# Kernel optimization log

Measured on AMD Instinct MI355X. Metric: run time of the kernel, lower is better.

The kernel has to match this reference:

```python
import jax, jax.numpy as jnp
import numpy as np
from jax import lax

DIM = 64        # Branch(dim)
OUT = 2048      # TimesBlock out_channels == TTT model_dim
NH = 8          # num_heads
HD = OUT // NH  # 256 head dim
INNER = 4 * HD  # ttt_mlp hidden
MB = 10         # mini_batch_size
BASE_LR = 0.1   # ttt_base_lr
NK = 6          # TimesBlock num_kernels (k = 1,3,5,7,9,11)
LN_EPS = 1e-6


def _gelu(x):
    return jax.nn.gelu(x, approximate=False)


def _gelu_bwd(x):
    return 0.5 * (1.0 + lax.erf(x / jnp.sqrt(2.0))) + x * jnp.exp(-0.5 * x * x) / jnp.sqrt(2.0 * jnp.pi)


def _ttt_head(qs, ks, vs, W1h, b1h, W2h, b2h, gw, gb):
    # qs/ks/vs: [NC, MB, HD]; sequential scan over mini-batch chunks (TTT inner GD)
    eta = BASE_LR / MB

    def step(carry, chunk):
        W1c, b1c, W2c, b2c = carry
        xq, xk, xv = chunk
        Z1 = xk @ W1c + b1c              # [MB, INNER]
        A1 = _gelu(Z1)
        Z2 = A1 @ W2c + b2c              # [MB, HD]
        # grad of 0.5*||LN(Z2) - (xv - xk)||^2 wrt Z2 (fused LN l2 backward)
        tgt = xv - xk
        mu = Z2.mean(-1, keepdims=True)
        std = jnp.sqrt(Z2.var(-1, keepdims=True) + LN_EPS)
        xhat = (2 * 0 + Z2 - mu) / std
        gout = (gw * xhat + gb) - tgt
        gxh = gout * gw
        gZ2 = (gxh - gxh.mean(-1, keepdims=True) - xhat * (gxh * xhat).mean(-1, keepdims=True)) / std
        gZ1 = (gZ2 @ W2c.T) * _gelu_bwd(Z1)
        # inner-model SGD step
        W1n = W1c - eta * (xk.T @ gZ1)
        b1n = b1c - eta * gZ1.sum(0)
        W2n = W2c - eta * (A1.T @ gZ2)
        b2n = b2c - eta * gZ2.sum(0)
        # apply updated inner model to queries, post-LN + residual
        Z1q = xq @ W1n + b1n
        Z2q = _gelu(Z1q) @ W2n + b2n
        muq = Z2q.mean(-1, keepdims=True)
        stdq = jnp.sqrt(Z2q.var(-1, keepdims=True) + LN_EPS)
        out = xq + gw * ((Z2q - muq) / stdq) + gb
        return (W1n, b1n, W2n, b2n), out

    _, outs = lax.scan(step, (W1h, b1h, W2h, b2h), (qs, ks, vs))
    return outs.reshape(-1, HD)  # [T, HD]


def _forward(x, seg, conv_ws, conv_bs, wq, wk, wv, wo, W1, b1, W2, b2, ln_w, ln_b):
    B, T, C = x.shape
    xg = jnp.transpose(x, (0, 2, 1)).reshape(B, C, T // seg, seg)
    dn = ('NCHW', 'OIHW', 'NCHW')
    acc = 0.0
    for w, bc in zip(conv_ws, conv_bs):
        acc = acc + lax.conv_general_dilated(xg, w, (1, 1), 'SAME', dimension_numbers=dn) + bc[None, :, None, None]
    xb = acc / float(len(conv_ws))            # TimesBlock: mean over kernel ensemble
    xb = jax.nn.silu(xb)
    xb = jnp.transpose(xb.reshape(B, OUT, T), (0, 2, 1))  # [B, T, OUT]

    def heads(h):  # [B,T,OUT] -> [B,NH,NC,MB,HD]
        return jnp.transpose(h.reshape(B, T, NH, HD), (0, 2, 1, 3)).reshape(B, NH, T // MB, MB, HD)

    q = heads(xb @ wq.T)
    k = heads(xb @ wk.T)
    v = heads(xb @ wv.T)
    f = jax.vmap(jax.vmap(_ttt_head, in_axes=(0, 0, 0, 0, 0, 0, 0, 0, 0)),
                 in_axes=(0, 0, 0, None, None, None, None, None, None))
    o = f(q, k, v, W1, b1, W2, b2, ln_w, ln_b)  # [B, NH, T, HD]
    o = jnp.transpose(o, (0, 2, 1, 3)).reshape(B, T, OUT)
    return o @ wo.T


def setup_inputs() -> dict:
    key = jax.random.key(0)
    ks = jax.random.split(key, 24)
    B, T = 2, 400
    inp = {"x": jax.random.normal(ks[0], (B, T, DIM), jnp.float32), "seg": 20}
    for i in range(NK):
        kk = 2 * i + 1
        fan_out = OUT * kk * kk
        inp[f"conv_w{i}"] = jax.random.normal(ks[1 + i], (OUT, DIM, kk, kk), jnp.float32) * np.sqrt(2.0 / fan_out)
        inp[f"conv_b{i}"] = jnp.zeros((OUT,), jnp.float32)
    for j, nm in enumerate(["wq", "wk", "wv", "wo"]):
        inp[nm] = jax.random.normal(ks[8 + j], (OUT, OUT), jnp.float32) * 0.02
    inp["W1"] = jax.random.normal(ks[12], (NH, HD, INNER), jnp.float32) * 0.02
    inp["b1"] = jnp.zeros((NH, INNER), jnp.float32)
    inp["W2"] = jax.random.normal(ks[13], (NH, INNER, HD), jnp.float32) * 0.02
    inp["b2"] = jnp.zeros((NH, HD), jnp.float32)
    inp["ln_w"] = jnp.ones((NH, HD), jnp.float32)
    inp["ln_b"] = jnp.zeros((NH, HD), jnp.float32)
    return inp


def reference(x, seg, conv_w0, conv_b0, conv_w1, conv_b1, conv_w2, conv_b2,
              conv_w3, conv_b3, conv_w4, conv_b4, conv_w5, conv_b5,
              wq, wk, wv, wo, W1, b1, W2, b2, ln_w, ln_b):
    conv_ws = [conv_w0, conv_w1, conv_w2, conv_w3, conv_w4, conv_w5]
    conv_bs = [conv_b0, conv_b1, conv_b2, conv_b3, conv_b4, conv_b5]
    return _forward(x, seg, conv_ws, conv_bs, wq, wk, wv, wo, W1, b1, W2, b2, ln_w, ln_b)
```

## Files before the change

kernel.cpp:

```cpp
#include <hip/hip_runtime.h>


typedef __bf16 bf16x8 __attribute__((ext_vector_type(8)));
typedef float  f32x4  __attribute__((ext_vector_type(4)));

__device__ __forceinline__ unsigned short f2bf(float f){
  unsigned int u = __builtin_bit_cast(unsigned int, f);
  u += 0x7fffu + ((u >> 16) & 1u);
  return (unsigned short)(u >> 16);
}
__device__ __forceinline__ float bf2f(unsigned short b){
  unsigned int u = ((unsigned int)b) << 16;
  return __builtin_bit_cast(float, u);
}
__device__ __forceinline__ float gelu_f(float x){
  return 0.5f * x * (1.0f + erff(x * 0.70710678118654752f));
}
__device__ __forceinline__ float gelu_bwd_f(float x){
  return 0.5f * (1.0f + erff(x * 0.70710678118654752f))
       + x * __expf(-0.5f * x * x) * 0.3989422804014327f;
}


__global__ __launch_bounds__(256) void k_weff(
    const float* __restrict__ w0, const float* __restrict__ w1,
    const float* __restrict__ w2, const float* __restrict__ w3,
    const float* __restrict__ w4, const float* __restrict__ w5,
    unsigned short* __restrict__ weff)
{
  extern __shared__ float sw[];
  const int off[6] = {0, 64, 640, 2240, 5376, 10560};
  const float* ws6[6] = {w0, w1, w2, w3, w4, w5};
  int o = blockIdx.x, tid = threadIdx.x;
#pragma unroll
  for (int i = 0; i < 6; i++){
    int kk = 2 * i + 1, sz = 64 * kk * kk;
    const float* src = ws6[i] + (size_t)o * sz;
    for (int idx = tid; idx < sz; idx += 256) sw[off[i] + idx] = src[idx];
  }
  __syncthreads();
  for (int t = tid; t < 7744; t += 256){
    int c = t / 121, dd = t % 121, di = dd / 11, dj = dd % 11;
    float s = 0.f;
#pragma unroll
    for (int i = 0; i < 6; i++){
      int kk = 2 * i + 1;
      int a = di - 5 + i, b = dj - 5 + i;
      if (a >= 0 && a < kk && b >= 0 && b < kk)
        s += sw[off[i] + (c * kk + a) * kk + b];
    }
    weff[(size_t)o * 7744 + t] = f2bf(s);
  }
}

__global__ __launch_bounds__(256) void k_im2col(
    const float* __restrict__ x, unsigned short* __restrict__ P)
{
  int idx = blockIdx.x * 256 + threadIdx.x;
  if (idx >= 800 * 7744) return;
  int n = idx / 7744, k = idx % 7744;
  int c = k / 121, dd = k % 121, di = dd / 11, dj = dd % 11;
  int b = n / 400, pos = n % 400, i = pos / 20, j = pos % 20;
  int ii = i + di - 5, jj = j + dj - 5;
  float v = 0.f;
  if (ii >= 0 && ii < 20 && jj >= 0 && jj < 20)
    v = x[((size_t)b * 400 + ii * 20 + jj) * 64 + c];
  P[idx] = f2bf(v);
}

__global__ __launch_bounds__(256) void k_wqkv(
    const float* __restrict__ wq, const float* __restrict__ wk,
    const float* __restrict__ wv, unsigned short* __restrict__ dst)
{
  int idx = blockIdx.x * 256 + threadIdx.x;
  if (idx >= 6144 * 2048) return;
  int m = idx >> 11, kk = idx & 2047;
  const float* src = (m < 2048) ? wq : ((m < 4096) ? wk : wv);
  dst[idx] = f2bf(src[(size_t)(m & 2047) * 2048 + kk]);
}

__global__ __launch_bounds__(256) void k_f2bf_copy(
    const float* __restrict__ src, unsigned short* __restrict__ dst, int n)
{
  int idx = blockIdx.x * 256 + threadIdx.x;
  if (idx < n) dst[idx] = f2bf(src[idx]);
}

__global__ __launch_bounds__(256) void k_bsum(
    const float* __restrict__ b0, const float* __restrict__ b1,
    const float* __restrict__ b2, const float* __restrict__ b3,
    const float* __restrict__ b4, const float* __restrict__ b5,
    float* __restrict__ bsum)
{
  int idx = blockIdx.x * 256 + threadIdx.x;
  if (idx < 2048)
    bsum[idx] = b0[idx] + b1[idx] + b2[idx] + b3[idx] + b4[idx] + b5[idx];
}

__global__ __launch_bounds__(256) void k_comb_silu(
    const float* __restrict__ p0, const float* __restrict__ p1,
    const float* __restrict__ bsum, unsigned short* __restrict__ xb)
{
  int i4 = (blockIdx.x * 256 + threadIdx.x) * 4;
  float4 a = *(const float4*)&p0[i4];
  float4 b = *(const float4*)&p1[i4];
  int mm = i4 & 2047;
  float4 bs = *(const float4*)&bsum[mm];
  float v[4] = {a.x + b.x + bs.x, a.y + b.y + bs.y, a.z + b.z + bs.z, a.w + b.w + bs.w};
  ushort4 o;
#pragma unroll
  for (int i = 0; i < 4; i++){
    float t = v[i] * (1.0f / 6.0f);
    float sv = t / (1.0f + __expf(-t));
    ((unsigned short*)&o)[i] = f2bf(sv);
  }
  *(ushort4*)&xb[i4] = o;
}

__global__ __launch_bounds__(256) void k_comb_add4(
    const float* __restrict__ p, float* __restrict__ out)
{
  int i4 = (blockIdx.x * 256 + threadIdx.x) * 4;
  float4 a = *(const float4*)&p[i4];
  float4 b = *(const float4*)&p[1638400 + i4];
  float4 c = *(const float4*)&p[3276800 + i4];
  float4 d = *(const float4*)&p[4915200 + i4];
  float4 o = {a.x + b.x + c.x + d.x, a.y + b.y + c.y + d.y,
              a.z + b.z + c.z + d.z, a.w + b.w + c.w + d.w};
  *(float4*)&out[i4] = o;
}

template<int MODE>
__global__ __launch_bounds__(256, 1) void k_gemm(
    const unsigned short* __restrict__ A, const unsigned short* __restrict__ B,
    int M, int N, int lda, int ldb, int kLen,
    unsigned short* __restrict__ qb, unsigned short* __restrict__ kb,
    unsigned short* __restrict__ vb, float* __restrict__ outf)
{
  __shared__ unsigned short As[128 * 32];
  __shared__ unsigned short Bs[128 * 32];
  int tid = threadIdx.x, w = tid >> 6, l = tid & 63, qd = l >> 4, lm = l & 15;
  int m0 = blockIdx.x * 128, n0 = blockIdx.y * 128;
  int kBase = blockIdx.z * kLen;

  f32x4 acc[4][4];
#pragma unroll
  for (int i = 0; i < 4; i++)
#pragma unroll
    for (int j = 0; j < 4; j++){ acc[i][j][0]=0.f; acc[i][j][1]=0.f; acc[i][j][2]=0.f; acc[i][j][3]=0.f; }

  int nk = kLen >> 5;
  for (int kt = 0; kt < nk; kt++){
    int k0 = kBase + (kt << 5);
#pragma unroll
    for (int i = 0; i < 2; i++){
      int cidx = tid + i * 256;
      int row = cidx >> 2, kc = (cidx & 3) << 3;
      *(uint4*)&As[row * 32 + kc] = *(const uint4*)&A[(size_t)(m0 + row) * lda + k0 + kc];
      int br = n0 + row; if (br >= N) br = N - 1;
      *(uint4*)&Bs[row * 32 + kc] = *(const uint4*)&B[(size_t)br * ldb + k0 + kc];
    }
    __syncthreads();
    bf16x8 af[4], bfv[4];
#pragma unroll
    for (int i = 0; i < 4; i++)
      af[i] = *(const bf16x8*)&As[((w >> 1) * 64 + i * 16 + lm) * 32 + qd * 8];
#pragma unroll
    for (int j = 0; j < 4; j++)
      bfv[j] = *(const bf16x8*)&Bs[((w & 1) * 64 + j * 16 + lm) * 32 + qd * 8];
#pragma unroll
    for (int i = 0; i < 4; i++)
#pragma unroll
      for (int j = 0; j < 4; j++)
        acc[i][j] = __builtin_amdgcn_mfma_f32_16x16x32_bf16(af[i], bfv[j], acc[i][j], 0, 0, 0);
    __syncthreads();
  }

#pragma unroll
  for (int i = 0; i < 4; i++){
    int mBase = m0 + (w >> 1) * 64 + i * 16 + qd * 4;
#pragma unroll
    for (int j = 0; j < 4; j++){
      int n = n0 + (w & 1) * 64 + j * 16 + lm;
      if (n < N){
#pragma unroll
        for (int rr = 0; rr < 4; rr++){
          float val = acc[i][j][rr];
          int mm = mBase + rr;
          if (MODE == 1){
            int proj = mm >> 11, o = mm & 2047, hh = o >> 8, d = o & 255;
            int bh = (n / 400) * 8 + hh, tt = n % 400;
            unsigned short* dst = (proj == 0) ? qb : ((proj == 1) ? kb : vb);
            dst[((size_t)bh * 400 + tt) * 256 + d] = f2bf(val);
          } else {
            outf[(size_t)blockIdx.z * M * N + (size_t)n * M + mm] = val;
          }
        }
      }
    }
  }
}

#define O_W1BT 0
#define O_W2K  16896
#define O_W2N  33792
#define O_XKQ  52224
#define O_TGT  54864
#define O_A1   57424
#define O_A1T  58144
#define O_GZ2  60192
#define O_GZ1  62832
#define O_XQ2  64880
#define O_GZ2T 67520
#define O_XKT  73664
#define O_A1Q  79808
#define O_F32  80528
#define O_GW   81168
#define O_GB   81424
#define US_TOTAL 81680
#define TTT_LDS_BYTES (81680 * 2)

#define A1T_IDX(r, c) (O_A1T + ((((r) * 32) + (c)) ^ (((r) & 3) << 3)))
#define GZ1_IDX(r, c) (O_GZ1 + ((((r) * 32) + (c)) ^ (((r) & 3) << 3)))

#define ETA 0.01f
#define BAR_STRIDE 32
#define PPAR 655360

__global__ __launch_bounds__(256, 1) void k_ttt(
    const unsigned short* __restrict__ qg, const unsigned short* __restrict__ kg,
    const unsigned short* __restrict__ vg,
    const float* __restrict__ W1g, const float* __restrict__ b1g,
    const float* __restrict__ W2g, const float* __restrict__ b2g,
    const float* __restrict__ gwg, const float* __restrict__ gbg,
    unsigned short* __restrict__ part, unsigned short* __restrict__ zqp,
    unsigned int* __restrict__ bar)
{
  extern __shared__ unsigned short lds[];
  float* ldsf = (float*)&lds[O_F32];

  int tid = threadIdx.x, w = tid >> 6, l = tid & 63, qd = l >> 4, lm = l & 15;
  int bid = blockIdx.x;
  int jj = bid >> 3, xx = bid & 7;
  int h  = xx + 8 * (jj >> 4);
  int sl = jj & 15;
  int hh = h & 7;

  for (int i = tid; i < US_TOTAL; i += 256) lds[i] = 0;
  __syncthreads();

  float w1r[4][4][4];
#pragma unroll
  for (int a = 0; a < 4; a++)
#pragma unroll
    for (int nt = 0; nt < 4; nt++)
#pragma unroll
      for (int rr = 0; rr < 4; rr++)
        w1r[a][nt][rr] = W1g[((size_t)hh * 256 + (4 * w + a) * 16 + qd * 4 + rr) * 1024
                             + sl * 64 + nt * 16 + lm];
  float w2r[16][4];
#pragma unroll
  for (int nt = 0; nt < 16; nt++)
#pragma unroll
    for (int rr = 0; rr < 4; rr++)
      w2r[nt][rr] = W2g[((size_t)hh * 1024 + sl * 64 + w * 16 + qd * 4 + rr) * 256
                        + nt * 16 + lm];
  if (tid < 64)  ldsf[tid] = b1g[hh * 1024 + sl * 64 + tid];
  if (tid < 256){
    ldsf[64 + tid] = b2g[hh * 256 + tid];
    lds[O_GW + tid] = f2bf(gwg[hh * 256 + tid]);
    lds[O_GB + tid] = f2bf(gbg[hh * 256 + tid]);
  }

#define WRITE_W1BF() do { \
  _Pragma("unroll") for (int a = 0; a < 4; a++){ \
    int m0i = (4 * w + a) * 16 + qd * 4; \
    _Pragma("unroll") for (int nt = 0; nt < 4; nt++){ \
      int n = nt * 16 + lm; \
      unsigned int p0 = f2bf(w1r[a][nt][0]) | ((unsigned int)f2bf(w1r[a][nt][1]) << 16); \
      unsigned int p1 = f2bf(w1r[a][nt][2]) | ((unsigned int)f2bf(w1r[a][nt][3]) << 16); \
      *(unsigned int*)&lds[O_W1BT + n * 264 + m0i]     = p0; \
      *(unsigned int*)&lds[O_W1BT + n * 264 + m0i + 2] = p1; \
    } } } while(0)

#define WRITE_W2BF() do { \
  int mB = w * 16 + qd * 4; \
  _Pragma("unroll") for (int nt = 0; nt < 16; nt++){ \
    int n = nt * 16 + lm; \
    _Pragma("unroll") for (int rr = 0; rr < 4; rr++) \
      lds[O_W2K + (mB + rr) * 264 + n] = f2bf(w2r[nt][rr]); \
    unsigned int p0 = f2bf(w2r[nt][0]) | ((unsigned int)f2bf(w2r[nt][1]) << 16); \
    unsigned int p1 = f2bf(w2r[nt][2]) | ((unsigned int)f2bf(w2r[nt][3]) << 16); \
    *(unsigned int*)&lds[O_W2N + n * 72 + mB]     = p0; \
    *(unsigned int*)&lds[O_W2N + n * 72 + mB + 2] = p1; \
  } } while(0)

  const size_t hb2 = (size_t)h * 400 * 256;

  unsigned int kreg[5], vreg[5];

#define LOAD_XK_REGS(NCH) do { \
  const unsigned int* kp = (const unsigned int*)(kg + hb2 + (size_t)(NCH) * 2560); \
  const unsigned int* vp = (const unsigned int*)(vg + hb2 + (size_t)(NCH) * 2560); \
  _Pragma("unroll") for (int i5 = 0; i5 < 5; i5++){ \
    kreg[i5] = kp[i5 * 256 + tid]; \
    vreg[i5] = vp[i5 * 256 + tid]; \
  } } while(0)

#define COMMIT_XK_TGT() do { \
  _Pragma("unroll") for (int i5 = 0; i5 < 5; i5++){ \
    int f2i = i5 * 256 + tid; \
    unsigned int ku = kreg[i5], vu = vreg[i5]; \
    int row = f2i >> 7, col = (f2i & 127) * 2; \
    *(unsigned int*)&lds[O_XKQ + row * 264 + col] = ku; \
    lds[O_XKT + col * 24 + row]       = (unsigned short)(ku & 0xffffu); \
    lds[O_XKT + (col + 1) * 24 + row] = (unsigned short)(ku >> 16); \
    float kv0 = bf2f((unsigned short)(ku & 0xffffu)), kv1 = bf2f((unsigned short)(ku >> 16)); \
    float vv0 = bf2f((unsigned short)(vu & 0xffffu)), vv1 = bf2f((unsigned short)(vu >> 16)); \
    unsigned int tu = (unsigned int)f2bf(vv0 - kv0) | ((unsigned int)f2bf(vv1 - kv1) << 16); \
    *(unsigned int*)&lds[O_TGT + row * 256 + col] = tu; \
  } } while(0)

#define LOAD_XQ(NCH) do { \
  const unsigned int* qp = (const unsigned int*)(qg + hb2 + (size_t)(NCH) * 2560); \
  _Pragma("unroll") for (int i5 = 0; i5 < 5; i5++){ \
    int f2i = i5 * 256 + tid; \
    unsigned int qu = qp[f2i]; \
    int row = f2i >> 7, col = (f2i & 127) * 2; \
    *(unsigned int*)&lds[O_XQ2 + row * 264 + col] = qu; \
  } } while(0)

  WRITE_W1BF();
  WRITE_W2BF();
  LOAD_XK_REGS(0);
  COMMIT_XK_TGT();
  LOAD_XQ(0);
  __syncthreads();

  for (int nch = 0; nch < 40; nch++){
    bf16x8 w1f[8];
#pragma unroll
    for (int ks = 0; ks < 8; ks++)
      w1f[ks] = *(const bf16x8*)&lds[O_W1BT + (w * 16 + lm) * 264 + ks * 32 + qd * 8];
    float b1n = ldsf[w * 16 + lm];

    f32x4 z1a; z1a[0]=0.f; z1a[1]=0.f; z1a[2]=0.f; z1a[3]=0.f;
#pragma unroll
    for (int ks = 0; ks < 8; ks++){
      bf16x8 av = *(const bf16x8*)&lds[O_XKQ + lm * 264 + ks * 32 + qd * 8];
      z1a = __builtin_amdgcn_mfma_f32_16x16x32_bf16(av, w1f[ks], z1a, 0, 0, 0);
    }
    float z1v[4];
#pragma unroll
    for (int rr = 0; rr < 4; rr++){
      z1v[rr] = z1a[rr] + b1n;
      int mr = qd * 4 + rr;
      if (mr < 10){
        float a1 = gelu_f(z1v[rr]);
        unsigned short ab = f2bf(a1);
        lds[O_A1 + mr * 72 + w * 16 + lm] = ab;
        lds[A1T_IDX(w * 16 + lm, mr)] = ab;
      }
    }
    __syncthreads();

    bf16x8 a1f[2], w2f[4][2];
#pragma unroll
    for (int ks = 0; ks < 2; ks++)
      a1f[ks] = *(const bf16x8*)&lds[O_A1 + lm * 72 + ks * 32 + qd * 8];
#pragma unroll
    for (int nt4 = 0; nt4 < 4; nt4++)
#pragma unroll
      for (int ks = 0; ks < 2; ks++)
        w2f[nt4][ks] = *(const bf16x8*)&lds[O_W2N + ((4 * w + nt4) * 16 + lm) * 72 + ks * 32 + qd * 8];

    {
      unsigned short* pslot = part + ((nch & 1) ? PPAR : 0) + (size_t)(h * 16 + sl) * 2560;
#pragma unroll
      for (int nt4 = 0; nt4 < 4; nt4++){
        int nt = 4 * w + nt4;
        f32x4 p; p[0]=0.f; p[1]=0.f; p[2]=0.f; p[3]=0.f;
#pragma unroll
        for (int ks = 0; ks < 2; ks++)
          p = __builtin_amdgcn_mfma_f32_16x16x32_bf16(a1f[ks], w2f[nt4][ks], p, 0, 0, 0);
#pragma unroll
        for (int rr = 0; rr < 4; rr++){
          int mr = qd * 4 + rr;
          if (mr < 10)
            __hip_atomic_store(&pslot[mr * 256 + nt * 16 + lm], f2bf(p[rr]),
                               __ATOMIC_RELAXED, __HIP_MEMORY_SCOPE_AGENT);
        }
      }
    }
    __syncthreads();

    if (tid == 0)
      __hip_atomic_fetch_add(bar + h * BAR_STRIDE, 1u, __ATOMIC_RELAXED, __HIP_MEMORY_SCOPE_AGENT);

    if (nch + 1 < 40)
      LOAD_XK_REGS(nch + 1);

    if (nch > 0){
      f32x4 zq; zq[0]=0.f; zq[1]=0.f; zq[2]=0.f; zq[3]=0.f;
#pragma unroll
      for (int ks = 0; ks < 8; ks++){
        bf16x8 av = *(const bf16x8*)&lds[O_XQ2 + lm * 264 + ks * 32 + qd * 8];
        zq = __builtin_amdgcn_mfma_f32_16x16x32_bf16(av, w1f[ks], zq, 0, 0, 0);
      }
#pragma unroll
      for (int rr = 0; rr < 4; rr++){
        int mr = qd * 4 + rr;
        if (mr < 10)
          lds[O_A1Q + mr * 72 + w * 16 + lm] = f2bf(gelu_f(zq[rr] + b1n));
      }
    }
    __syncthreads();

    if (nch > 0){
      LOAD_XQ(nch);
      unsigned short* zq_out = zqp + ((size_t)(h * 16 + sl) * 40 + (nch - 1)) * 2560;
      bf16x8 a1qf[2];
#pragma unroll
      for (int ks = 0; ks < 2; ks++)
        a1qf[ks] = *(const bf16x8*)&lds[O_A1Q + lm * 72 + ks * 32 + qd * 8];
#pragma unroll
      for (int nt4 = 0; nt4 < 4; nt4++){
        int nt = 4 * w + nt4;
        f32x4 p; p[0]=0.f; p[1]=0.f; p[2]=0.f; p[3]=0.f;
#pragma unroll
        for (int ks = 0; ks < 2; ks++)
          p = __builtin_amdgcn_mfma_f32_16x16x32_bf16(a1qf[ks], w2f[nt4][ks], p, 0, 0, 0);
        float bb = (sl == 0) ? ldsf[64 + nt * 16 + lm] : 0.f;
#pragma unroll
        for (int rr = 0; rr < 4; rr++){
          int mr = qd * 4 + rr;
          if (mr < 10)
            zq_out[mr * 256 + nt * 16 + lm] = f2bf(p[rr] + bb);
        }
      }
    }

    if (tid == 0){
      unsigned int target = 16u * (unsigned int)(nch + 1);
      unsigned int spins = 0;
      while (__hip_atomic_load(bar + h * BAR_STRIDE, __ATOMIC_RELAXED, __HIP_MEMORY_SCOPE_AGENT) < target
             && spins < 8000000u){ spins++; __builtin_amdgcn_s_sleep(1); }
    }
    __syncthreads();

    {
      const unsigned long long* pb = (const unsigned long long*)
          (part + ((nch & 1) ? PPAR : 0) + (size_t)h * 16 * 2560);
      for (int r2 = w; r2 < 10; r2 += 4){
        int c0 = l * 4;
        float zz[4];
#pragma unroll
        for (int i = 0; i < 4; i++) zz[i] = ldsf[64 + c0 + i];
#pragma unroll
        for (int s16 = 0; s16 < 16; s16++){
          unsigned long long u = __hip_atomic_load(&pb[(size_t)s16 * 640 + r2 * 64 + l],
                                                   __ATOMIC_RELAXED, __HIP_MEMORY_SCOPE_AGENT);
          zz[0] += bf2f((unsigned short)(u & 0xffffu));
          zz[1] += bf2f((unsigned short)((u >> 16) & 0xffffu));
          zz[2] += bf2f((unsigned short)((u >> 32) & 0xffffu));
          zz[3] += bf2f((unsigned short)(u >> 48));
        }
        float s1 = 0.f, s2 = 0.f;
#pragma unroll
        for (int i = 0; i < 4; i++){ s1 += zz[i]; s2 += zz[i] * zz[i]; }
#pragma unroll
        for (int off = 32; off >= 1; off >>= 1){ s1 += __shfl_xor(s1, off, 64); s2 += __shfl_xor(s2, off, 64); }
        float mu = s1 * (1.f / 256.f);
        float var = s2 * (1.f / 256.f) - mu * mu;
        float rstd = rsqrtf(var + 1e-6f);
        float xh[4], gx[4];
        float t1 = 0.f, t2 = 0.f;
#pragma unroll
        for (int i = 0; i < 4; i++){
          xh[i] = (zz[i] - mu) * rstd;
          float gwv = bf2f(lds[O_GW + c0 + i]), gbv = bf2f(lds[O_GB + c0 + i]);
          float tg = bf2f(lds[O_TGT + r2 * 256 + c0 + i]);
          float go = gwv * xh[i] + gbv - tg;
          gx[i] = go * gwv;
          t1 += gx[i]; t2 += gx[i] * xh[i];
        }
#pragma unroll
        for (int off = 32; off >= 1; off >>= 1){ t1 += __shfl_xor(t1, off, 64); t2 += __shfl_xor(t2, off, 64); }
        float m1 = t1 * (1.f / 256.f), m2 = t2 * (1.f / 256.f);
        float g0 = (gx[0] - m1 - xh[0] * m2) * rstd;
        float g1 = (gx[1] - m1 - xh[1] * m2) * rstd;
        float g2 = (gx[2] - m1 - xh[2] * m2) * rstd;
        float g3 = (gx[3] - m1 - xh[3] * m2) * rstd;
        unsigned int p0 = f2bf(g0) | ((unsigned int)f2bf(g1) << 16);
        unsigned int p1 = f2bf(g2) | ((unsigned int)f2bf(g3) << 16);
        *(unsigned int*)&lds[O_GZ2 + r2 * 264 + c0]     = p0;
        *(unsigned int*)&lds[O_GZ2 + r2 * 264 + c0 + 2] = p1;
      }
    }
    __syncthreads();

    {
      float sum = 0.f;
#pragma unroll
      for (int r2 = 0; r2 < 10; r2++){
        unsigned short g = lds[O_GZ2 + r2 * 264 + tid];
        lds[O_GZ2T + tid * 24 + r2] = g;
        sum += bf2f(g);
      }
      ldsf[64 + tid] -= ETA * sum;
    }
    {
      f32x4 g1a; g1a[0]=0.f; g1a[1]=0.f; g1a[2]=0.f; g1a[3]=0.f;
#pragma unroll
      for (int ks = 0; ks < 8; ks++){
        bf16x8 av = *(const bf16x8*)&lds[O_GZ2 + lm * 264 + ks * 32 + qd * 8];
        bf16x8 bv = *(const bf16x8*)&lds[O_W2K + (w * 16 + lm) * 264 + ks * 32 + qd * 8];
        g1a = __builtin_amdgcn_mfma_f32_16x16x32_bf16(av, bv, g1a, 0, 0, 0);
      }
#pragma unroll
      for (int rr = 0; rr < 4; rr++){
        int mr = qd * 4 + rr;
        if (mr < 10){
          float gz1 = g1a[rr] * gelu_bwd_f(z1v[rr]);
          lds[GZ1_IDX(w * 16 + lm, mr)] = f2bf(gz1);
        }
      }
    }
    __syncthreads();

    if (tid < 64){
      float sum = 0.f;
#pragma unroll
      for (int kx = 0; kx < 10; kx++) sum += bf2f(lds[GZ1_IDX(tid, kx)]);
      ldsf[tid] -= ETA * sum;
    }
#pragma unroll
    for (int a = 0; a < 4; a++){
      int mt = 4 * w + a;
      bf16x8 av = *(const bf16x8*)&lds[O_XKT + (mt * 16 + lm) * 24 + (qd & 1) * 8];
#pragma unroll
      for (int nt = 0; nt < 4; nt++){
        bf16x8 bv = *(const bf16x8*)&lds[GZ1_IDX(nt * 16 + lm, qd * 8)];
        f32x4 d; d[0]=0.f; d[1]=0.f; d[2]=0.f; d[3]=0.f;
        d = __builtin_amdgcn_mfma_f32_16x16x32_bf16(av, bv, d, 0, 0, 0);
#pragma unroll
        for (int rr = 0; rr < 4; rr++) w1r[a][nt][rr] -= ETA * d[rr];
      }
    }
    {
      bf16x8 av2 = *(const bf16x8*)&lds[A1T_IDX(w * 16 + lm, qd * 8)];
#pragma unroll
      for (int nt = 0; nt < 16; nt++){
        bf16x8 bv = *(const bf16x8*)&lds[O_GZ2T + (nt * 16 + lm) * 24 + (qd & 1) * 8];
        f32x4 d; d[0]=0.f; d[1]=0.f; d[2]=0.f; d[3]=0.f;
        d = __builtin_amdgcn_mfma_f32_16x16x32_bf16(av2, bv, d, 0, 0, 0);
#pragma unroll
        for (int rr = 0; rr < 4; rr++) w2r[nt][rr] -= ETA * d[rr];
      }
    }
    WRITE_W1BF();
    WRITE_W2BF();
    __syncthreads();

    if (nch + 1 < 40){
      COMMIT_XK_TGT();
    }
    __syncthreads();
  }

  {
    f32x4 zq; zq[0]=0.f; zq[1]=0.f; zq[2]=0.f; zq[3]=0.f;
#pragma unroll
    for (int ks = 0; ks < 8; ks++){
      bf16x8 av = *(const bf16x8*)&lds[O_XQ2 + lm * 264 + ks * 32 + qd * 8];
      bf16x8 bv = *(const bf16x8*)&lds[O_W1BT + (w * 16 + lm) * 264 + ks * 32 + qd * 8];
      zq = __builtin_amdgcn_mfma_f32_16x16x32_bf16(av, bv, zq, 0, 0, 0);
    }
    float b1n = ldsf[w * 16 + lm];
#pragma unroll
    for (int rr = 0; rr < 4; rr++){
      int mr = qd * 4 + rr;
      if (mr < 10)
        lds[O_A1Q + mr * 72 + w * 16 + lm] = f2bf(gelu_f(zq[rr] + b1n));
    }
  }
  __syncthreads();
  {
    unsigned short* zq_out = zqp + ((size_t)(h * 16 + sl) * 40 + 39) * 2560;
#pragma unroll
    for (int nt4 = 0; nt4 < 4; nt4++){
      int nt = 4 * w + nt4;
      f32x4 p; p[0]=0.f; p[1]=0.f; p[2]=0.f; p[3]=0.f;
#pragma unroll
      for (int ks = 0; ks < 2; ks++){
        bf16x8 av = *(const bf16x8*)&lds[O_A1Q + lm * 72 + ks * 32 + qd * 8];
        bf16x8 bv = *(const bf16x8*)&lds[O_W2N + (nt * 16 + lm) * 72 + ks * 32 + qd * 8];
        p = __builtin_amdgcn_mfma_f32_16x16x32_bf16(av, bv, p, 0, 0, 0);
      }
      float bb = (sl == 0) ? ldsf[64 + nt * 16 + lm] : 0.f;
#pragma unroll
      for (int rr = 0; rr < 4; rr++){
        int mr = qd * 4 + rr;
        if (mr < 10)
          zq_out[mr * 256 + nt * 16 + lm] = f2bf(p[rr] + bb);
      }
    }
  }
}

__global__ __launch_bounds__(256) void k_lnout(
    const unsigned short* __restrict__ zqp, const unsigned short* __restrict__ qg,
    const float* __restrict__ gwg, const float* __restrict__ gbg,
    unsigned short* __restrict__ obf)
{
  int w = threadIdx.x >> 6, l = threadIdx.x & 63;
  int gr = blockIdx.x * 4 + w;
  int h = gr / 400, t = gr % 400, hh = h & 7, b = h >> 3;
  int nch = t / 10, mr = t % 10;
  int c0 = l * 4;
  float z[4] = {0.f, 0.f, 0.f, 0.f};
#pragma unroll
  for (int sl = 0; sl < 16; sl++){
    const unsigned short* zp = zqp + (((size_t)(h * 16 + sl) * 40 + nch) * 10 + mr) * 256 + c0;
    ushort4 u = *(const ushort4*)zp;
    z[0] += bf2f(u.x); z[1] += bf2f(u.y); z[2] += bf2f(u.z); z[3] += bf2f(u.w);
  }
  float s1 = 0.f, s2 = 0.f;
#pragma unroll
  for (int i = 0; i < 4; i++){ s1 += z[i]; s2 += z[i] * z[i]; }
#pragma unroll
  for (int off = 32; off >= 1; off >>= 1){ s1 += __shfl_xor(s1, off, 64); s2 += __shfl_xor(s2, off, 64); }
  float mu = s1 * (1.f / 256.f);
  float var = s2 * (1.f / 256.f) - mu * mu;
  float rstd = rsqrtf(var + 1e-6f);
  const unsigned short* qp = &qg[((size_t)h * 400 + t) * 256];
  ushort4 qu = *(const ushort4*)&qp[c0];
  float qv[4] = {bf2f(qu.x), bf2f(qu.y), bf2f(qu.z), bf2f(qu.w)};
  unsigned short* op = &obf[((size_t)(b * 400 + t)) * 2048 + hh * 256];
#pragma unroll
  for (int i = 0; i < 4; i++){
    float xh = (z[i] - mu) * rstd;
    float o = qv[i] + gwg[hh * 256 + c0 + i] * xh + gbg[hh * 256 + c0 + i];
    op[c0 + i] = f2bf(o);
  }
}

#define WS_WEFF   0u
#define WS_P      31719424u
#define WS_WQKV   44109824u
#define WS_WOB    52428800u
#define WS_Z2ACC  62722048u
#define WS_XB     69275648u
#define WS_Q      72552448u
#define WS_K      75829248u
#define WS_V      79106048u
#define WS_OBF    82382848u
#define WS_BSUM   85659648u
#define WS_BAR    85667840u

extern "C" void kernel_launch(void* const* d_in, const int* in_sizes, int n_in,
                              void* d_out, int out_size, void* d_ws, size_t ws_size,
                              hipStream_t stream)
{
  (void)in_sizes; (void)n_in; (void)out_size; (void)ws_size;
  const float* x  = (const float*)d_in[0];
  const float* cw[6]; const float* cb[6];
  for (int i = 0; i < 6; i++){ cw[i] = (const float*)d_in[2 + 2 * i]; cb[i] = (const float*)d_in[3 + 2 * i]; }
  const float* wq  = (const float*)d_in[14];
  const float* wk  = (const float*)d_in[15];
  const float* wv  = (const float*)d_in[16];
  const float* wo  = (const float*)d_in[17];
  const float* W1  = (const float*)d_in[18];
  const float* b1  = (const float*)d_in[19];
  const float* W2  = (const float*)d_in[20];
  const float* b2  = (const float*)d_in[21];
  const float* lnw = (const float*)d_in[22];
  const float* lnb = (const float*)d_in[23];
  float* outf = (float*)d_out;

  char* wsb = (char*)d_ws;
  unsigned short* weff = (unsigned short*)(wsb + WS_WEFF);
  unsigned short* P    = (unsigned short*)(wsb + WS_P);
  unsigned short* wqkv = (unsigned short*)(wsb + WS_WQKV);
  unsigned short* wob  = (unsigned short*)(wsb + WS_WOB);
  unsigned short* xb   = (unsigned short*)(wsb + WS_XB);
  unsigned short* qb   = (unsigned short*)(wsb + WS_Q);
  unsigned short* kb   = (unsigned short*)(wsb + WS_K);
  unsigned short* vb   = (unsigned short*)(wsb + WS_V);
  unsigned short* part = (unsigned short*)(wsb + WS_Z2ACC);
  unsigned short* zqp = (unsigned short*)(wsb + WS_WEFF);
  unsigned short* obf = (unsigned short*)(wsb + WS_OBF);
  float* bsum = (float*)(wsb + WS_BSUM);
  unsigned int* bar = (unsigned int*)(wsb + WS_BAR);
  float* g0part = (float*)(wsb + WS_Q);
  float* g2part = (float*)(wsb + WS_WEFF);

  hipMemsetAsync(bar, 0, 16 * BAR_STRIDE * 4, stream);
  hipFuncSetAttribute(reinterpret_cast<const void*>(k_ttt),
                      hipFuncAttributeMaxDynamicSharedMemorySize, TTT_LDS_BYTES);
  hipFuncSetAttribute(reinterpret_cast<const void*>(k_weff),
                      hipFuncAttributeMaxDynamicSharedMemorySize, 18304 * 4);

  k_weff<<<2048, 256, 18304 * 4, stream>>>(cw[0], cw[1], cw[2], cw[3], cw[4], cw[5], weff);
  k_im2col<<<(800 * 7744 + 255) / 256, 256, 0, stream>>>(x, P);
  k_wqkv<<<(6144 * 2048 + 255) / 256, 256, 0, stream>>>(wq, wk, wv, wqkv);
  k_bsum<<<8, 256, 0, stream>>>(cb[0], cb[1], cb[2], cb[3], cb[4], cb[5], bsum);

  k_gemm<2><<<dim3(16, 7, 2), 256, 0, stream>>>(weff, P, 2048, 800, 7744, 7744, 3872,
                                                nullptr, nullptr, nullptr, g0part);
  k_comb_silu<<<1600, 256, 0, stream>>>(g0part, g0part + 1638400, bsum, xb);

  k_gemm<1><<<dim3(48, 7, 1), 256, 0, stream>>>(wqkv, xb, 6144, 800, 2048, 2048, 2048,
                                                qb, kb, vb, nullptr);

  k_f2bf_copy<<<(2048 * 2048 + 255) / 256, 256, 0, stream>>>(wo, wob, 2048 * 2048);

  k_ttt<<<256, 256, TTT_LDS_BYTES, stream>>>(qb, kb, vb, W1, b1, W2, b2, lnw, lnb,
                                             part, zqp, bar);
  k_lnout<<<1600, 256, 0, stream>>>(zqp, qb, lnw, lnb, obf);

  k_gemm<2><<<dim3(16, 7, 4), 256, 0, stream>>>(wob, obf, 2048, 800, 2048, 2048, 512,
                                                nullptr, nullptr, nullptr, g2part);
  k_comb_add4<<<1600, 256, 0, stream>>>(g2part, outf);
}
```

Baseline: 1.154 ms.

## Reduce TTT Z2 partials with fp32 global atomics instead of bf16 slot gather

The cross-block reduction of Z2 partial products inside the TTT kernel changes from each of 16 slices writing bf16 partials into double-buffered slots, then every block reading all 16 slots. Now each block atomically adds fp32 values into a per-chunk accumulator zeroed by a memset, and the reader loads one fp32 value per element. This cuts the 16-way gather reads per row and keeps the accumulation in fp32, at the cost of atomic contention, a larger buffer and an extra memset. It also folds the conv bias-sum kernel into k_weff to drop one launch.

```diff
diff --git a/kernel.cpp b/kernel.cpp
--- a/kernel.cpp
+++ b/kernel.cpp
@@ -21,17 +21,31 @@
        + x * __expf(-0.5f * x * x) * 0.3989422804014327f;
 }
 
+__device__ __forceinline__ float2 aload2(const float* p){
+  unsigned long long v = __hip_atomic_load((const unsigned long long*)p,
+                                           __ATOMIC_RELAXED, __HIP_MEMORY_SCOPE_AGENT);
+  union { unsigned long long u; float2 f; } cv; cv.u = v; return cv.f;
+}
+__device__ __forceinline__ void aadd(float* p, float v){
+  __hip_atomic_fetch_add(p, v, __ATOMIC_RELAXED, __HIP_MEMORY_SCOPE_AGENT);
+}
+
 
 __global__ __launch_bounds__(256) void k_weff(
     const float* __restrict__ w0, const float* __restrict__ w1,
     const float* __restrict__ w2, const float* __restrict__ w3,
     const float* __restrict__ w4, const float* __restrict__ w5,
-    unsigned short* __restrict__ weff)
+    const float* __restrict__ b0, const float* __restrict__ b1,
+    const float* __restrict__ b2, const float* __restrict__ b3,
+    const float* __restrict__ b4, const float* __restrict__ b5,
+    unsigned short* __restrict__ weff, float* __restrict__ bsum)
 {
   extern __shared__ float sw[];
   const int off[6] = {0, 64, 640, 2240, 5376, 10560};
   const float* ws6[6] = {w0, w1, w2, w3, w4, w5};
   int o = blockIdx.x, tid = threadIdx.x;
+  if (tid == 0)
+    bsum[o] = b0[o] + b1[o] + b2[o] + b3[o] + b4[o] + b5[o];
 #pragma unroll
   for (int i = 0; i < 6; i++){
     int kk = 2 * i + 1, sz = 64 * kk * kk;
@@ -84,17 +98,6 @@
 {
   int idx = blockIdx.x * 256 + threadIdx.x;
   if (idx < n) dst[idx] = f2bf(src[idx]);
-}
-
-__global__ __launch_bounds__(256) void k_bsum(
-    const float* __restrict__ b0, const float* __restrict__ b1,
-    const float* __restrict__ b2, const float* __restrict__ b3,
-    const float* __restrict__ b4, const float* __restrict__ b5,
-    float* __restrict__ bsum)
-{
-  int idx = blockIdx.x * 256 + threadIdx.x;
-  if (idx < 2048)
-    bsum[idx] = b0[idx] + b1[idx] + b2[idx] + b3[idx] + b4[idx] + b5[idx];
 }
 
 __global__ __launch_bounds__(256) void k_comb_silu(
@@ -225,7 +228,6 @@
 
 #define ETA 0.01f
 #define BAR_STRIDE 32
-#define PPAR 655360
 
 __global__ __launch_bounds__(256, 1) void k_ttt(
     const unsigned short* __restrict__ qg, const unsigned short* __restrict__ kg,
@@ -233,7 +235,7 @@
     const float* __restrict__ W1g, const float* __restrict__ b1g,
     const float* __restrict__ W2g, const float* __restrict__ b2g,
     const float* __restrict__ gwg, const float* __restrict__ gbg,
-    unsigned short* __restrict__ part, unsigned short* __restrict__ zqp,
+    float* __restrict__ z2acc, unsigned short* __restrict__ zqp,
     unsigned int* __restrict__ bar)
 {
   extern __shared__ unsigned short lds[];
@@ -338,6 +340,8 @@
   __syncthreads();
 
   for (int nch = 0; nch < 40; nch++){
+    const size_t chunkBase = (size_t)(h * 40 + nch) * 10 * 256;
+
     bf16x8 w1f[8];
 #pragma unroll
     for (int ks = 0; ks < 8; ks++)
@@ -374,22 +378,18 @@
       for (int ks = 0; ks < 2; ks++)
         w2f[nt4][ks] = *(const bf16x8*)&lds[O_W2N + ((4 * w + nt4) * 16 + lm) * 72 + ks * 32 + qd * 8];
 
-    {
-      unsigned short* pslot = part + ((nch & 1) ? PPAR : 0) + (size_t)(h * 16 + sl) * 2560;
-#pragma unroll
-      for (int nt4 = 0; nt4 < 4; nt4++){
-        int nt = 4 * w + nt4;
-        f32x4 p; p[0]=0.f; p[1]=0.f; p[2]=0.f; p[3]=0.f;
-#pragma unroll
-        for (int ks = 0; ks < 2; ks++)
-          p = __builtin_amdgcn_mfma_f32_16x16x32_bf16(a1f[ks], w2f[nt4][ks], p, 0, 0, 0);
-#pragma unroll
-        for (int rr = 0; rr < 4; rr++){
-          int mr = qd * 4 + rr;
-          if (mr < 10)
-            __hip_atomic_store(&pslot[mr * 256 + nt * 16 + lm], f2bf(p[rr]),
-                               __ATOMIC_RELAXED, __HIP_MEMORY_SCOPE_AGENT);
-        }
+#pragma unroll
+    for (int nt4 = 0; nt4 < 4; nt4++){
+      int nt = 4 * w + nt4;
+      f32x4 p; p[0]=0.f; p[1]=0.f; p[2]=0.f; p[3]=0.f;
+#pragma unroll
+      for (int ks = 0; ks < 2; ks++)
+        p = __builtin_amdgcn_mfma_f32_16x16x32_bf16(a1f[ks], w2f[nt4][ks], p, 0, 0, 0);
+#pragma unroll
+      for (int rr = 0; rr < 4; rr++){
+        int mr = qd * 4 + rr;
+        if (mr < 10)
+          aadd(&z2acc[chunkBase + (size_t)mr * 256 + nt * 16 + lm], p[rr]);
       }
     }
     __syncthreads();
@@ -448,54 +448,42 @@
     }
     __syncthreads();
 
-    {
-      const unsigned long long* pb = (const unsigned long long*)
-          (part + ((nch & 1) ? PPAR : 0) + (size_t)h * 16 * 2560);
-      for (int r2 = w; r2 < 10; r2 += 4){
-        int c0 = l * 4;
-        float zz[4];
-#pragma unroll
-        for (int i = 0; i < 4; i++) zz[i] = ldsf[64 + c0 + i];
-#pragma unroll
-        for (int s16 = 0; s16 < 16; s16++){
-          unsigned long long u = __hip_atomic_load(&pb[(size_t)s16 * 640 + r2 * 64 + l],
-                                                   __ATOMIC_RELAXED, __HIP_MEMORY_SCOPE_AGENT);
-          zz[0] += bf2f((unsigned short)(u & 0xffffu));
-          zz[1] += bf2f((unsigned short)((u >> 16) & 0xffffu));
-          zz[2] += bf2f((unsigned short)((u >> 32) & 0xffffu));
-          zz[3] += bf2f((unsigned short)(u >> 48));
-        }
-        float s1 = 0.f, s2 = 0.f;
-#pragma unroll
-        for (int i = 0; i < 4; i++){ s1 += zz[i]; s2 += zz[i] * zz[i]; }
-#pragma unroll
-        for (int off = 32; off >= 1; off >>= 1){ s1 += __shfl_xor(s1, off, 64); s2 += __shfl_xor(s2, off, 64); }
-        float mu = s1 * (1.f / 256.f);
-        float var = s2 * (1.f / 256.f) - mu * mu;
-        float rstd = rsqrtf(var + 1e-6f);
-        float xh[4], gx[4];
-        float t1 = 0.f, t2 = 0.f;
-#pragma unroll
-        for (int i = 0; i < 4; i++){
-          xh[i] = (zz[i] - mu) * rstd;
-          float gwv = bf2f(lds[O_GW + c0 + i]), gbv = bf2f(lds[O_GB + c0 + i]);
-          float tg = bf2f(lds[O_TGT + r2 * 256 + c0 + i]);
-          float go = gwv * xh[i] + gbv - tg;
-          gx[i] = go * gwv;
-          t1 += gx[i]; t2 += gx[i] * xh[i];
-        }
-#pragma unroll
-        for (int off = 32; off >= 1; off >>= 1){ t1 += __shfl_xor(t1, off, 64); t2 += __shfl_xor(t2, off, 64); }
-        float m1 = t1 * (1.f / 256.f), m2 = t2 * (1.f / 256.f);
-        float g0 = (gx[0] - m1 - xh[0] * m2) * rstd;
-        float g1 = (gx[1] - m1 - xh[1] * m2) * rstd;
-        float g2 = (gx[2] - m1 - xh[2] * m2) * rstd;
-        float g3 = (gx[3] - m1 - xh[3] * m2) * rstd;
-        unsigned int p0 = f2bf(g0) | ((unsigned int)f2bf(g1) << 16);
-        unsigned int p1 = f2bf(g2) | ((unsigned int)f2bf(g3) << 16);
-        *(unsigned int*)&lds[O_GZ2 + r2 * 264 + c0]     = p0;
-        *(unsigned int*)&lds[O_GZ2 + r2 * 264 + c0 + 2] = p1;
-      }
+    for (int r2 = w; r2 < 10; r2 += 4){
+      int c0 = l * 4;
+      const float* bp = &z2acc[chunkBase + (size_t)r2 * 256 + c0];
+      float2 u01 = aload2(bp);
+      float2 u23 = aload2(bp + 2);
+      float zz[4] = {u01.x, u01.y, u23.x, u23.y};
+      float s1 = 0.f, s2 = 0.f;
+#pragma unroll
+      for (int i = 0; i < 4; i++){ zz[i] += ldsf[64 + c0 + i]; s1 += zz[i]; s2 += zz[i] * zz[i]; }
+#pragma unroll
+      for (int off = 32; off >= 1; off >>= 1){ s1 += __shfl_xor(s1, off, 64); s2 += __shfl_xor(s2, off, 64); }
+      float mu = s1 * (1.f / 256.f);
+      float var = s2 * (1.f / 256.f) - mu * mu;
+      float rstd = rsqrtf(var + 1e-6f);
+      float xh[4], gx[4];
+      float t1 = 0.f, t2 = 0.f;
+#pragma unroll
+      for (int i = 0; i < 4; i++){
+        xh[i] = (zz[i] - mu) * rstd;
+        float gwv = bf2f(lds[O_GW + c0 + i]), gbv = bf2f(lds[O_GB + c0 + i]);
+        float tg = bf2f(lds[O_TGT + r2 * 256 + c0 + i]);
+        float go = gwv * xh[i] + gbv - tg;
+        gx[i] = go * gwv;
+        t1 += gx[i]; t2 += gx[i] * xh[i];
+      }
+#pragma unroll
+      for (int off = 32; off >= 1; off >>= 1){ t1 += __shfl_xor(t1, off, 64); t2 += __shfl_xor(t2, off, 64); }
+      float m1 = t1 * (1.f / 256.f), m2 = t2 * (1.f / 256.f);
+      float g0 = (gx[0] - m1 - xh[0] * m2) * rstd;
+      float g1 = (gx[1] - m1 - xh[1] * m2) * rstd;
+      float g2 = (gx[2] - m1 - xh[2] * m2) * rstd;
+      float g3 = (gx[3] - m1 - xh[3] * m2) * rstd;
+      unsigned int p0 = f2bf(g0) | ((unsigned int)f2bf(g1) << 16);
+      unsigned int p1 = f2bf(g2) | ((unsigned int)f2bf(g3) << 16);
+      *(unsigned int*)&lds[O_GZ2 + r2 * 264 + c0]     = p0;
+      *(unsigned int*)&lds[O_GZ2 + r2 * 264 + c0 + 2] = p1;
     }
     __syncthreads();
 
@@ -687,7 +675,7 @@
   unsigned short* qb   = (unsigned short*)(wsb + WS_Q);
   unsigned short* kb   = (unsigned short*)(wsb + WS_K);
   unsigned short* vb   = (unsigned short*)(wsb + WS_V);
-  unsigned short* part = (unsigned short*)(wsb + WS_Z2ACC);
+  float* z2acc = (float*)(wsb + WS_Z2ACC);
   unsigned short* zqp = (unsigned short*)(wsb + WS_WEFF);
   unsigned short* obf = (unsigned short*)(wsb + WS_OBF);
   float* bsum = (float*)(wsb + WS_BSUM);
@@ -701,10 +689,11 @@
   hipFuncSetAttribute(reinterpret_cast<const void*>(k_weff),
                       hipFuncAttributeMaxDynamicSharedMemorySize, 18304 * 4);
 
-  k_weff<<<2048, 256, 18304 * 4, stream>>>(cw[0], cw[1], cw[2], cw[3], cw[4], cw[5], weff);
+  k_weff<<<2048, 256, 18304 * 4, stream>>>(cw[0], cw[1], cw[2], cw[3], cw[4], cw[5],
+                                           cb[0], cb[1], cb[2], cb[3], cb[4], cb[5],
+                                           weff, bsum);
   k_im2col<<<(800 * 7744 + 255) / 256, 256, 0, stream>>>(x, P);
   k_wqkv<<<(6144 * 2048 + 255) / 256, 256, 0, stream>>>(wq, wk, wv, wqkv);
-  k_bsum<<<8, 256, 0, stream>>>(cb[0], cb[1], cb[2], cb[3], cb[4], cb[5], bsum);
 
   k_gemm<2><<<dim3(16, 7, 2), 256, 0, stream>>>(weff, P, 2048, 800, 7744, 7744, 3872,
                                                 nullptr, nullptr, nullptr, g0part);
@@ -714,9 +703,10 @@
                                                 qb, kb, vb, nullptr);
 
   k_f2bf_copy<<<(2048 * 2048 + 255) / 256, 256, 0, stream>>>(wo, wob, 2048 * 2048);
+  hipMemsetAsync(z2acc, 0, 16 * 40 * 10 * 256 * 4, stream);
 
   k_ttt<<<256, 256, TTT_LDS_BYTES, stream>>>(qb, kb, vb, W1, b1, W2, b2, lnw, lnb,
-                                             part, zqp, bar);
+                                             z2acc, zqp, bar);
   k_lnout<<<1600, 256, 0, stream>>>(zqp, qb, lnw, lnb, obf);
 
   k_gemm<2><<<dim3(16, 7, 4), 256, 0, stream>>>(wob, obf, 2048, 800, 2048, 2048, 512,
```

Result: faster. 1.033 ms (-10.5%).
